# Performance work log

Measured on AMD Instinct MI355X. Metric: run time of the kernel, lower is better.

## Reference

```python
import jax, jax.numpy as jnp
import numpy as np

TAU = 2.0
V_TH = 0.5
BN_EPS = 1e-5
ALPHA = 2.0  # spikingjelly surrogate.ATan default

@jax.custom_vjp
def spike_fn(x):
    # Heaviside forward, ATan surrogate backward (defined for fwdbwd parity)
    return (x >= 0.0).astype(x.dtype)

def _spike_fwd(x):
    return spike_fn(x), x

def _spike_bwd(x, g):
    return (g * (ALPHA / 2.0) / (1.0 + (jnp.pi / 2.0 * ALPHA * x) ** 2),)

spike_fn.defvjp(_spike_fwd, _spike_bwd)

def lif_multistep(x_seq):
    # MultiStepLIFNode: v <- v + (x - v)/tau ; spike = H(v - v_th) ; hard reset v<-v*(1-sg(spike))
    def step(v, x_t):
        v = v + (x_t - v) / TAU
        s = spike_fn(v - V_TH)
        v = v * (1.0 - jax.lax.stop_gradient(s))  # detach_reset=True, v_reset=0
        return v, s
    v0 = jnp.zeros_like(x_seq[0])
    _, spikes = jax.lax.scan(step, v0, x_seq)
    return spikes

def setup_inputs() -> dict:
    key = jax.random.key(0)
    k1, k2, k3 = jax.random.split(key, 3)
    T, B, N, D = 4, 64, 256, 512
    x = jax.random.normal(k1, (T, B, N, D), jnp.float32)
    mx = jax.random.normal(k2, (N, B, T, D), jnp.float32)
    W = jax.random.normal(k3, (D, D), jnp.float32) / np.sqrt(D).astype(np.float32)
    gamma = jnp.ones((D,), jnp.float32)
    beta = jnp.zeros((D,), jnp.float32)
    return {"x": x, "mx": mx, "W": W, "gamma": gamma, "beta": beta}

def reference(x, mx, W, gamma, beta):
    # mx: [N,B,T,D] -> transpose(0,2) -> [T,B,N,D]
    mxt = jnp.transpose(mx, (2, 1, 0, 3))
    # Linear (no bias): [T,B,N,D] @ W^T
    h = jnp.einsum('tbnd,ed->tbne', mxt, W)
    # BatchNorm1d(D) in training mode: stats over (T*B, N) per channel D (biased var)
    mean = h.mean(axis=(0, 1, 2))
    var = h.var(axis=(0, 1, 2))
    hn = (h - mean) * jax.lax.rsqrt(var + BN_EPS) * gamma + beta
    # LIF recurrence over T
    s = lif_multistep(hn)  # [T,B,N,D] binary spikes
    return x * s
```

## Files before the change

### kernel.cpp

```cpp
#include <hip/hip_runtime.h>
#include <math.h>

namespace {
constexpr int TDIM = 4, BDIM = 64, NDIM = 256, DDIM = 512;
constexpr int MROWS = 65536;
constexpr long long BND = 8388608LL;
constexpr double BN_EPS = 1e-5;

constexpr int BM = 64, BNT = 128, BK = 32;
constexpr int APITCH = BK + 2;
constexpr int WPITCH = BNT + 4;
constexpr int LDS_BYTES = (BM * APITCH + BK * WPITCH) * 8;

constexpr int BM3 = 128, BN3 = 64, BK3 = 16;
constexpr int AP3 = BM3 + 1;
constexpr int WP3 = BN3 + 1;

constexpr int NSA = 6, NSW = 5;
constexpr long long APL = 33554432LL;
constexpr long long WPL = 262144LL;
constexpr int CH8 = 22528;
}

typedef double d4 __attribute__((ext_vector_type(4)));
typedef int i32x4 __attribute__((ext_vector_type(4)));
typedef int i32x16 __attribute__((ext_vector_type(16)));

#define GLOAD16(g, d) __builtin_amdgcn_global_load_lds( \
    (const __attribute__((address_space(1))) void*)(g), \
    (__attribute__((address_space(3))) void*)(d), 16, 0, 0)

__global__ void init8_k(double* __restrict__ sums,
                        double* __restrict__ irow8, double* __restrict__ icol8)
{
    const int tid = threadIdx.x;
    sums[tid] = 0.0;
    sums[tid + 256] = 0.0;
    sums[tid + 512] = 0.0;
    sums[tid + 768] = 0.0;
    if (tid < 64) {
        const int l = tid;
        i32x16 z;
#pragma unroll
        for (int r = 0; r < 16; ++r) z[r] = 0;
        const int mb = (l & 31) * 0x01010101;
        const int ob = 0x01010101;
        i32x4 am = {mb, mb, mb, mb};
        i32x4 a1 = {ob, ob, ob, ob};
        i32x16 d1 = __builtin_amdgcn_mfma_i32_32x32x32_i8(am, a1, z, 0, 0, 0);
#pragma unroll
        for (int r = 0; r < 16; ++r)
            irow8[l * 16 + r] = (double)d1[r] / 32.0;
        i32x16 d2 = __builtin_amdgcn_mfma_i32_32x32x32_i8(a1, am, z, 0, 0, 0);
        icol8[l] = (double)d2[0] / 32.0;
    }
}

__global__ void init64_k(double* __restrict__ sums, double* __restrict__ rowmap)
{
    const int tid = threadIdx.x;
    sums[tid] = 0.0;
    sums[tid + 256] = 0.0;
    sums[tid + 512] = 0.0;
    sums[tid + 768] = 0.0;
    if (tid < 64) {
        const int l = tid;
        d4 z = {0.0, 0.0, 0.0, 0.0};
        d4 dr = __builtin_amdgcn_mfma_f64_16x16x4f64((double)(l & 15), 1.0, z, 0, 0, 0);
#pragma unroll
        for (int r = 0; r < 4; ++r)
            rowmap[l * 4 + r] = dr[r] * 0.25;
    }
}

__global__ void zero_k(double* sums)
{
    const int i = blockIdx.x * 256 + threadIdx.x;
    if (i < 1024) sums[i] = 0.0;
}

__global__ __launch_bounds__(256)
void slice_a_k(const float* __restrict__ src, char* __restrict__ dst)
{
    const int ri  = threadIdx.x & 63;
    const int ks0 = threadIdx.x >> 6;
    const long long row = (long long)blockIdx.x * 64 + ri;
#pragma unroll 1
    for (int it = 0; it < 8; ++it) {
        const int kseg = it * 4 + ks0;
        const float* sp = src + row * DDIM + kseg * 16;
        union { char c[16]; i32x4 v; } pk[NSA];
#pragma unroll
        for (int e = 0; e < 16; ++e) {
            const double V = (double)sp[e] * 4.0;
            const double u = rint(V);
            pk[0].c[e] = (char)(int)u;
            float r = (float)(V - u);
#pragma unroll
            for (int s = 1; s < NSA; ++s) {
                r *= 128.0f;
                const float uf = rintf(r);
                r -= uf;
                pk[s].c[e] = (char)(int)uf;
            }
        }
        const long long base = (long long)blockIdx.x * 32768 + kseg * 1024 + ri * 16;
#pragma unroll
        for (int s = 0; s < NSA; ++s)
            *(i32x4*)(dst + (long long)s * APL + base) = pk[s].v;
    }
}

__global__ __launch_bounds__(256)
void slice_w_k(const float* __restrict__ src, char* __restrict__ dst)
{
    const int cbk  = blockIdx.x >> 3;
    const int kgrp = blockIdx.x & 7;
    const int ci   = threadIdx.x & 63;
    const int kseg = kgrp * 4 + (threadIdx.x >> 6);
    const float* sp = src + (long long)(cbk * 64 + ci) * DDIM + kseg * 16;
    union { char c[16]; i32x4 v; } pk[NSW];
#pragma unroll
    for (int e = 0; e < 16; ++e) {
        const double V = (double)sp[e] * 256.0;
        const double u = rint(V);
        pk[0].c[e] = (char)(int)u;
        float r = (float)(V - u);
#pragma unroll
        for (int s = 1; s < NSW; ++s) {
            r *= 128.0f;
            const float uf = rintf(r);
            r -= uf;
            pk[s].c[e] = (char)(int)uf;
        }
    }
    const long long base = (long long)cbk * 32768 + kseg * 1024 + ci * 16;
#pragma unroll
    for (int s = 0; s < NSW; ++s)
        *(i32x4*)(dst + (long long)s * WPL + base) = pk[s].v;
}

template<int NW>
struct Stager {
    const char* gb[NW];
    int lo[NW];
    __device__ __forceinline__ void init(int w0, const char* Asl, const char* Wsl,
                                         long long aT, long long wT, int l)
    {
#pragma unroll
        for (int i = 0; i < NW; ++i) {
            const int idx = w0 + i;
            if (idx < 12) {
                gb[i] = Asl + (long long)(idx >> 1) * APL + aT
                      + (long long)(idx & 1) * 1024 + l * 16;
                lo[i] = (idx >> 1) * 2048 + (idx & 1) * 1024;
            } else {
                const int e = idx - 12;
                gb[i] = Wsl + (long long)(e >> 1) * WPL + wT
                      + (long long)(e & 1) * 1024 + l * 16;
                lo[i] = 12288 + (e >> 1) * 2048 + (e & 1) * 1024;
            }
        }
    }
    __device__ __forceinline__ void issue(char* buf, int ck)
    {
        const int go = ck * 2048;
#pragma unroll
        for (int i = 0; i < NW; ++i)
            GLOAD16(gb[i] + go, buf + lo[i]);
    }
};

template<int NW>
__device__ __forceinline__ void gemm8_loop(Stager<NW>& st, char* smb,
                                           i32x16 (&acc)[6], int roA, int roW,
                                           int c0)
{
#pragma unroll 2
    for (int c = 0; c < 16; ++c) {
        const char* bA = smb + (c & 1) * CH8;
        const char* bW = bA + 12288;
        i32x4 af[NSA], wf[NSW];
#pragma unroll
        for (int s = 0; s < NSA; ++s)
            af[s] = *(const i32x4*)(bA + s * 2048 + roA);
#pragma unroll
        for (int t = 0; t < NSW; ++t)
            wf[t] = *(const i32x4*)(bW + t * 2048 + roW);
#pragma unroll
        for (int s = 0; s < NSA; ++s)
#pragma unroll
            for (int t = 0; t < NSW; ++t)
                if (s + t <= 5)
                    acc[s + t] = __builtin_amdgcn_mfma_i32_32x32x32_i8(
                                     af[s], wf[t], acc[s + t], 0, 0, 0);
        if (c == 15) break;
        asm volatile("s_barrier" ::: "memory");
        if (c < 14) {
            st.issue(smb + (c & 1) * CH8, (c0 + c + 2) & 15);
            if constexpr (NW == 6)
                asm volatile("s_waitcnt vmcnt(6)" ::: "memory");
            else
                asm volatile("s_waitcnt vmcnt(5)" ::: "memory");
        } else {
            asm volatile("s_waitcnt vmcnt(0)" ::: "memory");
        }
        __builtin_amdgcn_sched_barrier(0);
        asm volatile("s_barrier" ::: "memory");
        __builtin_amdgcn_sched_barrier(0);
    }
}

__global__ __launch_bounds__(256, 3)
void gemm8_k(const char* __restrict__ Asl, const char* __restrict__ Wsl,
             double* __restrict__ hbuf, double* __restrict__ sums,
             const double* __restrict__ irow8, const double* __restrict__ icol8)
{
    __shared__ __align__(16) char sm[2][CH8];

    const int tid = threadIdx.x;
    const int bid = blockIdx.x;
    const int rb  = ((bid >> 6) << 3) | (bid & 7);
    const int cb  = (bid >> 3) & 7;

    const int c0 = (((bid >> 6) * 5) + ((bid & 7) * 3)) & 15;

    const int w  = tid >> 6;
    const int l  = tid & 63;
    const int wr = w >> 1;
    const int wc = w & 1;

    const long long aTile = (long long)rb * 32768;
    const long long wTile = (long long)cb * 32768;

    i32x16 acc[6];
#pragma unroll
    for (int g = 0; g < 6; ++g)
#pragma unroll
        for (int r = 0; r < 16; ++r) acc[g][r] = 0;

    const int roA = (l >> 5) * 1024 + (32 * wr + (l & 31)) * 16;
    const int roW = (l >> 5) * 1024 + (32 * wc + (l & 31)) * 16;

    char* smb = &sm[0][0];
    if (w < 2) {
        Stager<6> st;
        st.init(6 * w, Asl, Wsl, aTile, wTile, l);
        st.issue(smb, c0);
        st.issue(smb + CH8, (c0 + 1) & 15);
        asm volatile("s_waitcnt vmcnt(6)" ::: "memory");
        __builtin_amdgcn_sched_barrier(0);
        asm volatile("s_barrier" ::: "memory");
        __builtin_amdgcn_sched_barrier(0);
        gemm8_loop<6>(st, smb, acc, roA, roW, c0);
    } else {
        Stager<5> st;
        st.init(12 + 5 * (w - 2), Asl, Wsl, aTile, wTile, l);
        st.issue(smb, c0);
        st.issue(smb + CH8, (c0 + 1) & 15);
        asm volatile("s_waitcnt vmcnt(5)" ::: "memory");
        __builtin_amdgcn_sched_barrier(0);
        asm volatile("s_barrier" ::: "memory");
        __builtin_amdgcn_sched_barrier(0);
        gemm8_loop<5>(st, smb, acc, roA, roW, c0);
    }

    int irw[16];
#pragma unroll
    for (int r = 0; r < 16; ++r) irw[r] = (int)irow8[l * 16 + r];
    const int icl = (int)icol8[l];

    const double C7 = 1.0 / 128.0, CMB = 1.0 / 1024.0;
    double lsum = 0.0, lsq = 0.0;
    const int colg = cb * 64 + 32 * wc + icl;
    const int row0 = rb * 64 + 32 * wr;
#pragma unroll
    for (int r = 0; r < 16; ++r) {
        double t = (double)acc[5][r];
        t = fma(t, C7, (double)acc[4][r]);
        t = fma(t, C7, (double)acc[3][r]);
        t = fma(t, C7, (double)acc[2][r]);
        t = fma(t, C7, (double)acc[1][r]);
        t = fma(t, C7, (double)acc[0][r]);
        const double h = t * CMB;
        hbuf[(size_t)(row0 + irw[r]) * DDIM + colg] = h;
        lsum += h;
        lsq = fma(h, h, lsq);
    }

    __syncthreads();
    double* Ss = (double*)sm;
    const int ctr = wr * 2 + (l >> 5);
    const int cloc = 32 * wc + icl;
    Ss[cloc * 4 + ctr] = lsum;
    Ss[256 + cloc * 4 + ctr] = lsq;
    __syncthreads();
    if (tid < 64) {
        double s = 0.0, q = 0.0;
#pragma unroll
        for (int k = 0; k < 4; ++k) {
            s += Ss[tid * 4 + k];
            q += Ss[256 + tid * 4 + k];
        }
        atomicAdd(&sums[cb * 64 + tid], s);
        atomicAdd(&sums[512 + cb * 64 + tid], q);
    }
}

__global__ __launch_bounds__(256, 2)
void gemm3_k(const float* __restrict__ mx, const float* __restrict__ Wm,
             double* __restrict__ hbuf, double* __restrict__ sums,
             const double* __restrict__ rowmap)
{
    __shared__ double Atr[BK3 * AP3];
    __shared__ double Wt [BK3 * WP3];

    const int tid = threadIdx.x;
    const int bid = blockIdx.x;
    const int rb  = ((bid >> 6) << 3) | (bid & 7);
    const int cb  = (bid >> 3) & 7;
    const int row0 = rb * BM3;
    const int col0 = cb * BN3;

    const int w  = tid >> 6;
    const int l  = tid & 63;
    const int wr = w >> 1;
    const int wc = w & 1;
    const int lr = l & 15;
    const int kq = l >> 4;

    int irow[4];
#pragma unroll
    for (int r = 0; r < 4; ++r)
        irow[r] = (int)rowmap[l * 4 + r];

    const int arow = tid >> 1;
    const int af   = (tid & 1) * 8;
    const int wrow = tid >> 2;
    const int wf   = (tid & 3) * 4;
    const float* aSrc = mx + (size_t)(row0 + arow) * DDIM + af;
    const float* wSrc = Wm + (size_t)(col0 + wrow) * DDIM + wf;

    d4 acc[4][2];
#pragma unroll
    for (int i = 0; i < 4; ++i)
#pragma unroll
        for (int j = 0; j < 2; ++j) acc[i][j] = (d4){0.0, 0.0, 0.0, 0.0};

    float4 pa0 = *(const float4*)(aSrc + 0);
    float4 pa1 = *(const float4*)(aSrc + 4);
    float4 pw  = *(const float4*)(wSrc + 0);

    for (int kk = 0; kk < DDIM; kk += BK3) {
        __syncthreads();
        Atr[(af + 0) * AP3 + arow] = (double)pa0.x;
        Atr[(af + 1) * AP3 + arow] = (double)pa0.y;
        Atr[(af + 2) * AP3 + arow] = (double)pa0.z;
        Atr[(af + 3) * AP3 + arow] = (double)pa0.w;
        Atr[(af + 4) * AP3 + arow] = (double)pa1.x;
        Atr[(af + 5) * AP3 + arow] = (double)pa1.y;
        Atr[(af + 6) * AP3 + arow] = (double)pa1.z;
        Atr[(af + 7) * AP3 + arow] = (double)pa1.w;
        Wt[(wf + 0) * WP3 + wrow] = (double)pw.x;
        Wt[(wf + 1) * WP3 + wrow] = (double)pw.y;
        Wt[(wf + 2) * WP3 + wrow] = (double)pw.z;
        Wt[(wf + 3) * WP3 + wrow] = (double)pw.w;
        __syncthreads();

        if (kk + BK3 < DDIM) {
            pa0 = *(const float4*)(aSrc + kk + BK3 + 0);
            pa1 = *(const float4*)(aSrc + kk + BK3 + 4);
            pw  = *(const float4*)(wSrc + kk + BK3 + 0);
        }

#pragma unroll
        for (int ks = 0; ks < BK3 / 4; ++ks) {
            const int kabs = ks * 4 + kq;
            double a[4], b[2];
#pragma unroll
            for (int i = 0; i < 4; ++i)
                a[i] = Atr[kabs * AP3 + 64 * wr + 16 * i + lr];
#pragma unroll
            for (int j = 0; j < 2; ++j)
                b[j] = Wt[kabs * WP3 + 32 * wc + 16 * j + lr];
#pragma unroll
            for (int i = 0; i < 4; ++i)
#pragma unroll
                for (int j = 0; j < 2; ++j)
                    acc[i][j] = __builtin_amdgcn_mfma_f64_16x16x4f64(
                                    a[i], b[j], acc[i][j], 0, 0, 0);
        }
    }

#pragma unroll
    for (int i = 0; i < 4; ++i) {
#pragma unroll
        for (int j = 0; j < 2; ++j) {
            const size_t cbase = (size_t)col0 + 32 * wc + 16 * j + lr;
            const size_t rbase = (size_t)row0 + 64 * wr + 16 * i;
#pragma unroll
            for (int r = 0; r < 4; ++r)
                hbuf[(rbase + irow[r]) * DDIM + cbase] = acc[i][j][r];
        }
    }

    __syncthreads();
    double* Ssum = Atr;
    double* Ssq  = Atr + 512;
    const int ctr = wr * 4 + kq;
#pragma unroll
    for (int j = 0; j < 2; ++j) {
        const int cloc = 32 * wc + 16 * j + lr;
        double s = 0.0, q = 0.0;
#pragma unroll
        for (int i = 0; i < 4; ++i)
#pragma unroll
            for (int r = 0; r < 4; ++r) {
                const double v = acc[i][j][r];
                s += v;
                q = fma(v, v, q);
            }
        Ssum[cloc * 8 + ctr] = s;
        Ssq [cloc * 8 + ctr] = q;
    }
    __syncthreads();
    if (tid < 64) {
        double s = 0.0, q = 0.0;
#pragma unroll
        for (int c = 0; c < 8; ++c) {
            s += Ssum[tid * 8 + c];
            q += Ssq [tid * 8 + c];
        }
        atomicAdd(&sums[col0 + tid], s);
        atomicAdd(&sums[512 + col0 + tid], q);
    }
}

template<int MODE>
__global__ __launch_bounds__(256)
void gemm_k(const float* __restrict__ mx, const float* __restrict__ Wm,
            double* __restrict__ hbuf, double* __restrict__ sums,
            const double* __restrict__ scale, const double* __restrict__ shiftv,
            const float* __restrict__ x, float* __restrict__ out)
{
    __shared__ __align__(16) char smem[LDS_BYTES];
    double (*Ald)[APITCH] = reinterpret_cast<double(*)[APITCH]>(smem);
    double (*Wld)[WPITCH] = reinterpret_cast<double(*)[WPITCH]>(smem + (size_t)BM * APITCH * 8);

    const int tid  = threadIdx.x;
    const int rb   = blockIdx.x >> 2;
    const int cb   = blockIdx.x & 3;
    const int row0 = rb * BM;
    const int col0 = cb * BNT;

    const int arow = tid >> 2;
    const int ak   = (tid & 3) * 8;
    const int erow = tid >> 1;
    const int wk   = (tid & 1) * 16;

    const float* aSrc = mx + (size_t)(row0 + arow) * DDIM;
    const float* wSrc = Wm + (size_t)(col0 + erow) * DDIM;

    const int rg = tid >> 4;
    const int cg = tid & 15;

    double acc[4][8];
#pragma unroll
    for (int i = 0; i < 4; ++i)
#pragma unroll
        for (int j = 0; j < 8; ++j) acc[i][j] = 0.0;

    for (int kk = 0; kk < DDIM; kk += BK) {
        const float4 a0 = *(const float4*)(aSrc + kk + ak);
        const float4 a1 = *(const float4*)(aSrc + kk + ak + 4);
        const float4 w0 = *(const float4*)(wSrc + kk + wk);
        const float4 w1 = *(const float4*)(wSrc + kk + wk + 4);
        const float4 w2 = *(const float4*)(wSrc + kk + wk + 8);
        const float4 w3 = *(const float4*)(wSrc + kk + wk + 12);
        __syncthreads();
        Ald[arow][ak + 0] = (double)a0.x; Ald[arow][ak + 1] = (double)a0.y;
        Ald[arow][ak + 2] = (double)a0.z; Ald[arow][ak + 3] = (double)a0.w;
        Ald[arow][ak + 4] = (double)a1.x; Ald[arow][ak + 5] = (double)a1.y;
        Ald[arow][ak + 6] = (double)a1.z; Ald[arow][ak + 7] = (double)a1.w;
        const float wfv[16] = {w0.x, w0.y, w0.z, w0.w, w1.x, w1.y, w1.z, w1.w,
                               w2.x, w2.y, w2.z, w2.w, w3.x, w3.y, w3.z, w3.w};
#pragma unroll
        for (int q = 0; q < 16; ++q) Wld[wk + q][erow] = (double)wfv[q];
        __syncthreads();

#pragma unroll 4
        for (int d = 0; d < BK; ++d) {
            double a[4], wv[8];
#pragma unroll
            for (int i = 0; i < 4; ++i) a[i] = Ald[rg * 4 + i][d];
#pragma unroll
            for (int j = 0; j < 8; ++j) wv[j] = Wld[d][cg * 8 + j];
#pragma unroll
            for (int i = 0; i < 4; ++i)
#pragma unroll
                for (int j = 0; j < 8; ++j)
                    acc[i][j] = fma(a[i], wv[j], acc[i][j]);
        }
    }

    if (MODE <= 1) {
        __syncthreads();
        double* scr = reinterpret_cast<double*>(smem);
#pragma unroll
        for (int j = 0; j < 8; ++j) {
            const double s = acc[0][j] + acc[1][j] + acc[2][j] + acc[3][j];
            const double q = acc[0][j]*acc[0][j] + acc[1][j]*acc[1][j]
                           + acc[2][j]*acc[2][j] + acc[3][j]*acc[3][j];
            scr[(cg * 8 + j) * 16 + rg] = s;
            scr[2048 + (cg * 8 + j) * 16 + rg] = q;
        }
        __syncthreads();
        if (tid < 128) {
            double s = 0.0, q = 0.0;
#pragma unroll
            for (int r = 0; r < 16; ++r) {
                s += scr[tid * 16 + r];
                q += scr[2048 + tid * 16 + r];
            }
            atomicAdd(&sums[col0 + tid], s);
            atomicAdd(&sums[512 + col0 + tid], q);
        }
    }

    if (MODE == 2) {
        const int p  = rb * 16 + rg;
        const int nn = p >> 6;
        const int bb = p & 63;
#pragma unroll
        for (int j = 0; j < 8; ++j) {
            const int e = col0 + cg * 8 + j;
            const double sc = scale[e];
            const double sh = shiftv[e];
            const size_t basex = (size_t)bb * (NDIM * DDIM) + (size_t)nn * DDIM + e;
            double v = 0.0;
#pragma unroll
            for (int t = 0; t < 4; ++t) {
                const double hn = fma(acc[t][j], sc, sh);
                v = v + (hn - v) / 2.0;
                const bool s = (v - 0.5) >= 0.0;
                const size_t xi = (size_t)t * BND + basex;
                out[xi] = s ? x[xi] : 0.0f;
                if (s) v = 0.0;
            }
        }
    }
}

__global__ void stat_k(const double* __restrict__ sums,
                       const float* __restrict__ gamma, const float* __restrict__ beta,
                       double* __restrict__ scale, double* __restrict__ shiftv)
{
    const int e = blockIdx.x * 256 + threadIdx.x;
    if (e < 512) {
        const double mean = sums[e] * (1.0 / 65536.0);
        const double msq  = sums[512 + e] * (1.0 / 65536.0);
        const double var  = msq - mean * mean;
        const double inv  = 1.0 / sqrt(var + BN_EPS);
        const double g    = (double)gamma[e] * inv;
        scale[e]  = g;
        shiftv[e] = (double)beta[e] - mean * g;
    }
}

__global__ __launch_bounds__(256)
void lifh_k(const double* __restrict__ hbuf, const double* __restrict__ scale,
            const double* __restrict__ shiftv, const float* __restrict__ x,
            float* __restrict__ out)
{
    const size_t i = (size_t)blockIdx.x * 256 + threadIdx.x;
    const int e4 = (int)(i & 127) * 4;
    const size_t p = i >> 7;
    const int nn = (int)(p >> 6);
    const int bb = (int)(p & 63);
    double sc[4], sh[4], v[4];
#pragma unroll
    for (int j = 0; j < 4; ++j) {
        sc[j] = scale[e4 + j];
        sh[j] = shiftv[e4 + j];
        v[j] = 0.0;
    }
    const double* hp = hbuf + p * 2048 + e4;
    const size_t basex = (size_t)bb * (NDIM * DDIM) + (size_t)nn * DDIM + e4;
#pragma unroll
    for (int t = 0; t < 4; ++t) {
        const double2 ha = *(const double2*)(hp + (size_t)t * 512);
        const double2 hb = *(const double2*)(hp + (size_t)t * 512 + 2);
        const double hv[4] = {ha.x, ha.y, hb.x, hb.y};
        const size_t xi = (size_t)t * BND + basex;
        const float4 xv = *(const float4*)(x + xi);
        const float xf[4] = {xv.x, xv.y, xv.z, xv.w};
        float of[4];
#pragma unroll
        for (int j = 0; j < 4; ++j) {
            const double hn = fma(hv[j], sc[j], sh[j]);
            v[j] = v[j] + (hn - v[j]) / 2.0;
            const bool s = (v[j] - 0.5) >= 0.0;
            of[j] = s ? xf[j] : 0.0f;
            if (s) v[j] = 0.0;
        }
        float4 ov; ov.x = of[0]; ov.y = of[1]; ov.z = of[2]; ov.w = of[3];
        *(float4*)(out + xi) = ov;
    }
}

extern "C" void kernel_launch(void* const* d_in, const int* in_sizes, int n_in,
                              void* d_out, int out_size, void* d_ws, size_t ws_size,
                              hipStream_t stream)
{
    const float* x     = (const float*)d_in[0];
    const float* mx    = (const float*)d_in[1];
    const float* Wm    = (const float*)d_in[2];
    const float* gamma = (const float*)d_in[3];
    const float* beta  = (const float*)d_in[4];
    float* out = (float*)d_out;

    char* ws = (char*)d_ws;
    double* sums   = (double*)ws;
    double* scale  = (double*)(ws + 8192);
    double* shiftv = scale + 512;
    double* rowmap = (double*)(ws + 16384);
    double* irow8  = (double*)(ws + 18432);
    double* icol8  = (double*)(ws + 26624);
    double* hbuf   = (double*)(ws + 32768);

    const size_t HBSZ   = (size_t)MROWS * DDIM * 8;
    const size_t OFF_AS = 32768 + HBSZ;
    const size_t ASSZ   = (size_t)NSA * APL;
    const size_t OFF_WS = OFF_AS + ASSZ;
    const size_t WSSZ   = (size_t)NSW * WPL;
    const size_t need8  = OFF_WS + WSSZ;
    const size_t need_h = 32768 + HBSZ;

    if (ws_size >= need8) {
        char* Asl = ws + OFF_AS;
        char* Wsl = ws + OFF_WS;
        hipLaunchKernelGGL(init8_k, dim3(1), dim3(256), 0, stream,
                           sums, irow8, icol8);
        hipLaunchKernelGGL(slice_w_k, dim3(64), dim3(256), 0, stream, Wm, Wsl);
        hipLaunchKernelGGL(slice_a_k, dim3(1024), dim3(256), 0, stream, mx, Asl);
        hipLaunchKernelGGL(gemm8_k, dim3(8192), dim3(256), 0, stream,
                           Asl, Wsl, hbuf, sums, irow8, icol8);
        hipLaunchKernelGGL(stat_k, dim3(2), dim3(256), 0, stream,
                           sums, gamma, beta, scale, shiftv);
        hipLaunchKernelGGL(lifh_k, dim3(8192), dim3(256), 0, stream,
                           hbuf, scale, shiftv, x, out);
    } else if (ws_size >= need_h) {
        hipLaunchKernelGGL(init64_k, dim3(1), dim3(256), 0, stream, sums, rowmap);
        hipLaunchKernelGGL(gemm3_k, dim3(4096), dim3(256), 0, stream,
                           mx, Wm, hbuf, sums, rowmap);
        hipLaunchKernelGGL(stat_k, dim3(2), dim3(256), 0, stream,
                           sums, gamma, beta, scale, shiftv);
        hipLaunchKernelGGL(lifh_k, dim3(8192), dim3(256), 0, stream,
                           hbuf, scale, shiftv, x, out);
    } else {
        hipLaunchKernelGGL(zero_k, dim3(4), dim3(256), 0, stream, sums);
        hipLaunchKernelGGL((gemm_k<0>), dim3(4096), dim3(256), 0, stream,
                           mx, Wm, nullptr, sums, nullptr, nullptr, nullptr, nullptr);
        hipLaunchKernelGGL(stat_k, dim3(2), dim3(256), 0, stream,
                           sums, gamma, beta, scale, shiftv);
        hipLaunchKernelGGL((gemm_k<2>), dim3(4096), dim3(256), 0, stream,
                           mx, Wm, nullptr, nullptr, scale, shiftv, x, out);
    }
}
```

Before: 479.0 us.

## Load W fragments directly into registers instead of staging through LDS

Each wave now loads its own W slices for the int8 split GEMM from global memory into registers, and only A chunks are staged in LDS with double-buffered global_load_lds. This shrinks LDS use and removes the W LDS reads. In exchange, W is fetched only one chunk ahead and the waitcnt forces those loads to finish each iteration, which may expose global latency. W data that waves sharing a column used to share through LDS is now loaded redundantly.

```diff
diff --git a/kernel.cpp b/kernel.cpp
--- a/kernel.cpp
+++ b/kernel.cpp
@@ -19,7 +19,7 @@
 constexpr int NSA = 6, NSW = 5;
 constexpr long long APL = 33554432LL;
 constexpr long long WPL = 262144LL;
-constexpr int CH8 = 22528;
+constexpr int ABUF = 12288;
 }
 
 typedef double d4 __attribute__((ext_vector_type(4)));
@@ -140,89 +140,40 @@
         *(i32x4*)(dst + (long long)s * WPL + base) = pk[s].v;
 }
 
-template<int NW>
-struct Stager {
-    const char* gb[NW];
-    int lo[NW];
-    __device__ __forceinline__ void init(int w0, const char* Asl, const char* Wsl,
-                                         long long aT, long long wT, int l)
+struct StagerA {
+    const char* gb[3];
+    int lo[3];
+    __device__ __forceinline__ void init(int w, const char* Asl,
+                                         long long aT, int l)
     {
 #pragma unroll
-        for (int i = 0; i < NW; ++i) {
-            const int idx = w0 + i;
-            if (idx < 12) {
-                gb[i] = Asl + (long long)(idx >> 1) * APL + aT
-                      + (long long)(idx & 1) * 1024 + l * 16;
-                lo[i] = (idx >> 1) * 2048 + (idx & 1) * 1024;
-            } else {
-                const int e = idx - 12;
-                gb[i] = Wsl + (long long)(e >> 1) * WPL + wT
-                      + (long long)(e & 1) * 1024 + l * 16;
-                lo[i] = 12288 + (e >> 1) * 2048 + (e & 1) * 1024;
-            }
+        for (int i = 0; i < 3; ++i) {
+            const int idx = 3 * w + i;
+            const int s = idx >> 1, j = idx & 1;
+            gb[i] = Asl + (long long)s * APL + aT + (long long)j * 1024 + l * 16;
+            lo[i] = s * 2048 + j * 1024;
         }
     }
     __device__ __forceinline__ void issue(char* buf, int ck)
     {
         const int go = ck * 2048;
 #pragma unroll
-        for (int i = 0; i < NW; ++i)
+        for (int i = 0; i < 3; ++i)
             GLOAD16(gb[i] + go, buf + lo[i]);
     }
 };
-
-template<int NW>
-__device__ __forceinline__ void gemm8_loop(Stager<NW>& st, char* smb,
-                                           i32x16 (&acc)[6], int roA, int roW,
-                                           int c0)
-{
-#pragma unroll 2
-    for (int c = 0; c < 16; ++c) {
-        const char* bA = smb + (c & 1) * CH8;
-        const char* bW = bA + 12288;
-        i32x4 af[NSA], wf[NSW];
-#pragma unroll
-        for (int s = 0; s < NSA; ++s)
-            af[s] = *(const i32x4*)(bA + s * 2048 + roA);
-#pragma unroll
-        for (int t = 0; t < NSW; ++t)
-            wf[t] = *(const i32x4*)(bW + t * 2048 + roW);
-#pragma unroll
-        for (int s = 0; s < NSA; ++s)
-#pragma unroll
-            for (int t = 0; t < NSW; ++t)
-                if (s + t <= 5)
-                    acc[s + t] = __builtin_amdgcn_mfma_i32_32x32x32_i8(
-                                     af[s], wf[t], acc[s + t], 0, 0, 0);
-        if (c == 15) break;
-        asm volatile("s_barrier" ::: "memory");
-        if (c < 14) {
-            st.issue(smb + (c & 1) * CH8, (c0 + c + 2) & 15);
-            if constexpr (NW == 6)
-                asm volatile("s_waitcnt vmcnt(6)" ::: "memory");
-            else
-                asm volatile("s_waitcnt vmcnt(5)" ::: "memory");
-        } else {
-            asm volatile("s_waitcnt vmcnt(0)" ::: "memory");
-        }
-        __builtin_amdgcn_sched_barrier(0);
-        asm volatile("s_barrier" ::: "memory");
-        __builtin_amdgcn_sched_barrier(0);
-    }
-}
 
 __global__ __launch_bounds__(256, 3)
 void gemm8_k(const char* __restrict__ Asl, const char* __restrict__ Wsl,
              double* __restrict__ hbuf, double* __restrict__ sums,
              const double* __restrict__ irow8, const double* __restrict__ icol8)
 {
-    __shared__ __align__(16) char sm[2][CH8];
+    __shared__ __align__(16) char sm[2 * ABUF];
 
     const int tid = threadIdx.x;
     const int bid = blockIdx.x;
     const int rb  = ((bid >> 6) << 3) | (bid & 7);
     const int cb  = (bid >> 3) & 7;
-
     const int c0 = (((bid >> 6) * 5) + ((bid & 7) * 3)) & 15;
 
     const int w  = tid >> 6;
@@ -231,7 +182,9 @@
     const int wc = w & 1;
 
     const long long aTile = (long long)rb * 32768;
-    const long long wTile = (long long)cb * 32768;
+    const long long wLane = (long long)cb * 32768
+                          + (long long)(l >> 5) * 1024
+                          + (long long)(32 * wc + (l & 31)) * 16;
 
     i32x16 acc[6];
 #pragma unroll
@@ -240,29 +193,55 @@
         for (int r = 0; r < 16; ++r) acc[g][r] = 0;
 
     const int roA = (l >> 5) * 1024 + (32 * wr + (l & 31)) * 16;
-    const int roW = (l >> 5) * 1024 + (32 * wc + (l & 31)) * 16;
-
-    char* smb = &sm[0][0];
-    if (w < 2) {
-        Stager<6> st;
-        st.init(6 * w, Asl, Wsl, aTile, wTile, l);
-        st.issue(smb, c0);
-        st.issue(smb + CH8, (c0 + 1) & 15);
-        asm volatile("s_waitcnt vmcnt(6)" ::: "memory");
+
+    StagerA st;
+    st.init(w, Asl, aTile, l);
+
+    i32x4 wreg[5];
+
+#pragma unroll
+    for (int t = 0; t < 5; ++t)
+        wreg[t] = *(const i32x4*)(Wsl + (long long)t * WPL + wLane
+                                  + (long long)c0 * 2048);
+    st.issue(sm, c0);
+    st.issue(sm + ABUF, (c0 + 1) & 15);
+    asm volatile("s_waitcnt vmcnt(3)" ::: "memory");
+    __builtin_amdgcn_sched_barrier(0);
+    asm volatile("s_barrier" ::: "memory");
+    __builtin_amdgcn_sched_barrier(0);
+
+#pragma unroll 2
+    for (int c = 0; c < 16; ++c) {
+        const char* bA = sm + (c & 1) * ABUF;
+        i32x4 af[NSA];
+#pragma unroll
+        for (int s = 0; s < NSA; ++s)
+            af[s] = *(const i32x4*)(bA + s * 2048 + roA);
+#pragma unroll
+        for (int s = 0; s < NSA; ++s)
+#pragma unroll
+            for (int t = 0; t < NSW; ++t)
+                if (s + t <= 5)
+                    acc[s + t] = __builtin_amdgcn_mfma_i32_32x32x32_i8(
+                                     af[s], wreg[t], acc[s + t], 0, 0, 0);
+        if (c == 15) break;
+        asm volatile("s_barrier" ::: "memory");
+        {
+            const int ck1 = (c0 + c + 1) & 15;
+#pragma unroll
+            for (int t = 0; t < 5; ++t)
+                wreg[t] = *(const i32x4*)(Wsl + (long long)t * WPL + wLane
+                                          + (long long)ck1 * 2048);
+        }
+        if (c < 14) {
+            st.issue(sm + (c & 1) * ABUF, (c0 + c + 2) & 15);
+            asm volatile("s_waitcnt vmcnt(3)" ::: "memory");
+        } else {
+            asm volatile("s_waitcnt vmcnt(0)" ::: "memory");
+        }
         __builtin_amdgcn_sched_barrier(0);
         asm volatile("s_barrier" ::: "memory");
         __builtin_amdgcn_sched_barrier(0);
-        gemm8_loop<6>(st, smb, acc, roA, roW, c0);
-    } else {
-        Stager<5> st;
-        st.init(12 + 5 * (w - 2), Asl, Wsl, aTile, wTile, l);
-        st.issue(smb, c0);
-        st.issue(smb + CH8, (c0 + 1) & 15);
-        asm volatile("s_waitcnt vmcnt(5)" ::: "memory");
-        __builtin_amdgcn_sched_barrier(0);
-        asm volatile("s_barrier" ::: "memory");
-        __builtin_amdgcn_sched_barrier(0);
-        gemm8_loop<5>(st, smb, acc, roA, roW, c0);
     }
 
     int irw[16];
```

New measurement: 512.4 us. +7.0%, slower.
